# Kernel optimization log

Hardware: AMD Instinct MI355X
Metric: run time of the kernel (lower is better)

## Reference

```python
import jax, jax.numpy as jnp
import numpy as np

N = 100000
E = 1600000
F_IN = 128
HID = 256
C_OUT = 4


def setup_inputs() -> dict:
    key = jax.random.key(0)
    ks = jax.random.split(key, 8)
    x = jax.random.normal(ks[0], (N, F_IN), dtype=jnp.float32)
    edge_index = jax.random.randint(ks[1], (2, E), 0, N, dtype=jnp.int64)
    s1 = 1.0 / np.sqrt(F_IN)
    s2 = 1.0 / np.sqrt(HID)
    # PyG SAGEConv: lin_l (applied to aggregated neighbors, has bias), lin_r (root, no bias)
    w1_l = jax.random.uniform(ks[2], (HID, F_IN), jnp.float32, -s1, s1)
    w1_r = jax.random.uniform(ks[3], (HID, F_IN), jnp.float32, -s1, s1)
    b1 = jax.random.uniform(ks[4], (HID,), jnp.float32, -s1, s1)
    w2_l = jax.random.uniform(ks[5], (C_OUT, HID), jnp.float32, -s2, s2)
    w2_r = jax.random.uniform(ks[6], (C_OUT, HID), jnp.float32, -s2, s2)
    b2 = jax.random.uniform(ks[7], (C_OUT,), jnp.float32, -s2, s2)
    return {"x": x, "edge_index": edge_index, "w1_l": w1_l, "w1_r": w1_r,
            "b1": b1, "w2_l": w2_l, "w2_r": w2_r, "b2": b2}


def _mean_agg(h, src, dst, inv_deg):
    # gather source features, scatter-sum to targets, divide by in-degree
    summed = jax.ops.segment_sum(h[src], dst, num_segments=N)
    return summed * inv_deg[:, None]


def _sage_conv(h, src, dst, inv_deg, w_l, w_r, b):
    agg = _mean_agg(h, src, dst, inv_deg)
    return agg @ w_l.T + b + h @ w_r.T


def reference(x, edge_index, w1_l, w1_r, b1, w2_l, w2_r, b2):
    src, dst = edge_index[0], edge_index[1]
    deg = jax.ops.segment_sum(jnp.ones((E,), jnp.float32), dst, num_segments=N)
    inv_deg = jnp.where(deg > 0, 1.0 / jnp.maximum(deg, 1.0), 0.0)
    h = _sage_conv(x, src, dst, inv_deg, w1_l, w1_r, b1)
    h = jax.nn.relu(h)
    # dropout is identity in eval mode
    h = _sage_conv(h, src, dst, inv_deg, w2_l, w2_r, b2)
    return jax.nn.log_softmax(h, axis=1)
```

## Files before the change

### kernel.cpp

```cpp
#include <hip/hip_runtime.h>

#define N_NODES 100000
#define N_ROWS_PAD 100032
#define N_EDGES 1600000
#define F_IN    128
#define HID     256
#define C_OUT   4

#define NB 391
#define EPT 16
#define SLACK 8192

#define GEMM_BLOCKS 256
#define NTASKS 6252

typedef short short8v __attribute__((ext_vector_type(8)));
typedef unsigned short u16x8 __attribute__((ext_vector_type(8)));
typedef float f32x4 __attribute__((ext_vector_type(4)));

__device__ __forceinline__ ushort f2b(float f) {
    union { float f; unsigned u; } v; v.f = f;
    unsigned u = v.u;
    return (ushort)((u + 0x7FFFu + ((u >> 16) & 1u)) >> 16);
}
__device__ __forceinline__ float b2f(ushort u) {
    union { unsigned u; float f; } v; v.u = ((unsigned)u) << 16; return v.f;
}

__device__ __forceinline__ void gload16(const void* g, void* l) {
    __builtin_amdgcn_global_load_lds(
        (const __attribute__((address_space(1))) unsigned int*)g,
        (__attribute__((address_space(3))) unsigned int*)l, 16, 0, 0);
}

template <int CTRL>
__device__ __forceinline__ float dpp_radd(float x) {
    int y = __builtin_amdgcn_update_dpp(0, __float_as_int(x), CTRL, 0xf, 0xf, true);
    return x + __int_as_float(y);
}
__device__ __forceinline__ float row16_sum(float x) {
    x = dpp_radd<0x128>(x);
    x = dpp_radd<0x124>(x);
    x = dpp_radd<0x122>(x);
    x = dpp_radd<0x121>(x);
    return x;
}

__global__ void k_binit(int* __restrict__ bcur) {
    int t = blockIdx.x * 256 + threadIdx.x;
    if (t < 512) bcur[t] = t * SLACK;
}

__global__ __launch_bounds__(256) void k_bucket(const int* __restrict__ ei,
                                                int* __restrict__ bcur,
                                                int* __restrict__ ebuf) {
    __shared__ int hist[NB];
    __shared__ int sbase[NB];
    int t = threadIdx.x;
    for (int i = t; i < NB; i += 256) hist[i] = 0;
    __syncthreads();
    int pk[EPT], bkt[EPT], lofs[EPT];
    int base = blockIdx.x * (256 * EPT);
    #pragma unroll
    for (int i = 0; i < EPT; ++i) {
        int e = base + i * 256 + t;
        if (e < N_EDGES) {
            int s = ei[e], d = ei[N_EDGES + e];
            pk[i] = s | ((d & 255) << 20);
            bkt[i] = d >> 8;
            lofs[i] = atomicAdd(&hist[bkt[i]], 1);
        } else bkt[i] = -1;
    }
    __syncthreads();
    for (int i = t; i < NB; i += 256) {
        int h = hist[i];
        sbase[i] = h ? atomicAdd(&bcur[i], h) : 0;
    }
    __syncthreads();
    #pragma unroll
    for (int i = 0; i < EPT; ++i) {
        if (bkt[i] >= 0)
            ebuf[sbase[bkt[i]] + lofs[i]] = pk[i];
    }
}

__global__ void k_bscan(const int* __restrict__ bcur, int* __restrict__ boff) {
    __shared__ int sh[512];
    int t = threadIdx.x;
    int v = (t < NB) ? (bcur[t] - t * SLACK) : 0;
    sh[t] = v;
    __syncthreads();
    #pragma unroll
    for (int off = 1; off < 512; off <<= 1) {
        int add = (t >= off) ? sh[t - off] : 0;
        __syncthreads();
        sh[t] += add;
        __syncthreads();
    }
    boff[t] = sh[t] - v;
}

__global__ __launch_bounds__(256) void k_place(const int* __restrict__ boff,
                                               const int* __restrict__ ebuf,
                                               int* __restrict__ rowptr,
                                               float* __restrict__ inv_deg,
                                               int* __restrict__ csr_src) {
    __shared__ int eld[SLACK];
    __shared__ int ldeg[256];
    __shared__ int sh[256];
    __shared__ int lcur[256];
    int b = blockIdx.x, t = threadIdx.x;
    int e0 = boff[b];
    int cnt = boff[b + 1] - e0;
    const int* src = ebuf + (size_t)b * SLACK;
    for (int i = t; i < cnt; i += 256) eld[i] = src[i];
    ldeg[t] = 0;
    __syncthreads();
    for (int i = t; i < cnt; i += 256)
        atomicAdd(&ldeg[(eld[i] >> 20) & 255], 1);
    __syncthreads();
    int v = ldeg[t];
    sh[t] = v;
    __syncthreads();
    #pragma unroll
    for (int off = 1; off < 256; off <<= 1) {
        int add = (t >= off) ? sh[t - off] : 0;
        __syncthreads();
        sh[t] += add;
        __syncthreads();
    }
    int start = e0 + sh[t] - v;
    int node = b * 256 + t;
    if (node < N_NODES) {
        rowptr[node] = start;
        inv_deg[node] = (v > 0) ? 1.0f / (float)v : 0.0f;
    }
    if (b == 0 && t == 0) rowptr[N_NODES] = N_EDGES;
    lcur[t] = start;
    __syncthreads();
    for (int i = t; i < cnt; i += 256) {
        int ev = eld[i];
        int pos = atomicAdd(&lcur[(ev >> 20) & 255], 1);
        csr_src[pos] = ev & 0xFFFFF;
    }
}

__global__ void k_xcast(const float* __restrict__ x, ushort* __restrict__ abf) {
    int t = blockIdx.x * 256 + threadIdx.x;
    float4 xv = *(const float4*)(x + (size_t)t * 4);
    int row = t >> 5;
    int colq = (t & 31) * 4;
    ushort4 o; o.x = f2b(xv.x); o.y = f2b(xv.y); o.z = f2b(xv.z); o.w = f2b(xv.w);
    *(ushort4*)(abf + (size_t)row * 256 + 128 + colq) = o;
}

__global__ void k_wbf(const float* __restrict__ w1l, const float* __restrict__ w1r,
                      const float* __restrict__ w2l, const float* __restrict__ w2r,
                      ushort* __restrict__ wbf, float* __restrict__ w2t) {
    int i = blockIdx.x * 256 + threadIdx.x;
    int col = i >> 8, k = i & 255;
    float v = (k < 128) ? w1l[col * 128 + k] : w1r[col * 128 + (k - 128)];
    wbf[i] = f2b(v);
    if (i < 256) {
        #pragma unroll
        for (int c = 0; c < 4; ++c) {
            w2t[i * 8 + c]     = w2l[c * HID + i];
            w2t[i * 8 + 4 + c] = w2r[c * HID + i];
        }
    }
}

__global__ void k_aggregate(const int* __restrict__ rowptr, const int* __restrict__ csr_src,
                            const float* __restrict__ inv_deg, ushort* __restrict__ abf) {
    int lane = threadIdx.x & 63;
    int v = blockIdx.x * 4 + (threadIdx.x >> 6);
    if (v >= N_NODES) return;
    int r0 = rowptr[v], r1 = rowptr[v + 1];
    int q = lane >> 4, li = lane & 15;
    float a0[8], a1[8];
    #pragma unroll
    for (int j = 0; j < 8; ++j) { a0[j] = 0.f; a1[j] = 0.f; }
    int e = r0 + q;
    for (; e + 4 < r1; e += 8) {
        int s0 = csr_src[e];
        int s1 = csr_src[e + 4];
        u16x8 u0 = *(const u16x8*)(abf + (size_t)s0 * 256 + 128 + li * 8);
        u16x8 u1 = *(const u16x8*)(abf + (size_t)s1 * 256 + 128 + li * 8);
        #pragma unroll
        for (int j = 0; j < 8; ++j) { a0[j] += b2f(u0[j]); a1[j] += b2f(u1[j]); }
    }
    if (e < r1) {
        int s0 = csr_src[e];
        u16x8 u0 = *(const u16x8*)(abf + (size_t)s0 * 256 + 128 + li * 8);
        #pragma unroll
        for (int j = 0; j < 8; ++j) a0[j] += b2f(u0[j]);
    }
    #pragma unroll
    for (int j = 0; j < 8; ++j) {
        float s = a0[j] + a1[j];
        s += __shfl_xor(s, 16);
        s += __shfl_xor(s, 32);
        a0[j] = s;
    }
    if (q == 0) {
        float id = inv_deg[v];
        u16x8 o;
        #pragma unroll
        for (int j = 0; j < 8; ++j) o[j] = f2b(a0[j] * id);
        *(u16x8*)(abf + (size_t)v * 256 + li * 8) = o;
    }
}

__global__ __launch_bounds__(256, 1) void k_mfma(
    const ushort* __restrict__ abf, const ushort* __restrict__ wbf,
    const float* __restrict__ b1, const float* __restrict__ w2t,
    float* __restrict__ zb, float* __restrict__ rb)
{
    __shared__ ushort bufB[16 * 8 * 512];

    int t = threadIdx.x;
    int w = t >> 6, l = t & 63;
    int lr = l & 15, lk = l >> 4;

    #pragma unroll
    for (int j = 0; j < 32; ++j) {
        int sb = w * 32 + j;
        int n = sb >> 3, kc = sb & 7;
        gload16(wbf + (size_t)(n * 16 + lr) * 256 + kc * 32 + lk * 8,
                &bufB[sb * 512]);
    }
    __syncthreads();

    int wid = blockIdx.x * 4 + w;
    int ps = (int)(((unsigned)wid * NTASKS) >> 10);
    int pe = (int)(((unsigned)(wid + 1) * NTASKS) >> 10);

    for (int p = ps; p < pe; ++p) {
        size_t r0 = (size_t)p * 16;
        short8v af[8];
        const ushort* a0 = abf + (r0 + lr) * 256 + lk * 8;
        #pragma unroll
        for (int kc = 0; kc < 8; ++kc)
            af[kc] = *(const short8v*)(a0 + kc * 32);
        __builtin_amdgcn_sched_barrier(0);

        f32x4 acc[16] = {};
        #pragma unroll
        for (int kc = 0; kc < 8; ++kc) {
            #pragma unroll
            for (int n = 0; n < 8; ++n) {
                short8v bf = *(const short8v*)&bufB[(n * 8 + kc) * 512 + l * 8];
                acc[n] = __builtin_amdgcn_mfma_f32_16x16x32_bf16(af[kc], bf, acc[n], 0, 0, 0);
            }
            __builtin_amdgcn_sched_barrier(0);
            #pragma unroll
            for (int n = 8; n < 16; ++n) {
                short8v bf = *(const short8v*)&bufB[(n * 8 + kc) * 512 + l * 8];
                acc[n] = __builtin_amdgcn_mfma_f32_16x16x32_bf16(af[kc], bf, acc[n], 0, 0, 0);
            }
            __builtin_amdgcn_sched_barrier(0);
        }

        float pz[4][8];
        #pragma unroll
        for (int q = 0; q < 4; ++q)
            #pragma unroll
            for (int c = 0; c < 8; ++c) pz[q][c] = 0.f;
        #pragma unroll
        for (int n = 0; n < 16; ++n) {
            int col = n * 16 + lr;
            float bias = b1[col];
            f32x4 wa = *(const f32x4*)(w2t + col * 8);
            f32x4 wb = *(const f32x4*)(w2t + col * 8 + 4);
            #pragma unroll
            for (int q = 0; q < 4; ++q) {
                float h = fmaxf(acc[n][q] + bias, 0.f);
                pz[q][0] += h * wa[0]; pz[q][1] += h * wa[1];
                pz[q][2] += h * wa[2]; pz[q][3] += h * wa[3];
                pz[q][4] += h * wb[0]; pz[q][5] += h * wb[1];
                pz[q][6] += h * wb[2]; pz[q][7] += h * wb[3];
            }
        }
        __builtin_amdgcn_sched_barrier(0);
        #pragma unroll
        for (int q = 0; q < 4; ++q)
            #pragma unroll
            for (int c = 0; c < 8; ++c)
                pz[q][c] = row16_sum(pz[q][c]);
        if (lr == 0) {
            #pragma unroll
            for (int q = 0; q < 4; ++q) {
                size_t row = r0 + lk * 4 + q;
                if (row < N_NODES) {
                    *(float4*)(zb + row * 4) = make_float4(pz[q][0], pz[q][1], pz[q][2], pz[q][3]);
                    *(float4*)(rb + row * 4) = make_float4(pz[q][4], pz[q][5], pz[q][6], pz[q][7]);
                }
            }
        }
    }
}

__global__ void k_final(const float* __restrict__ zb, const float* __restrict__ rb,
                        const int* __restrict__ rowptr, const int* __restrict__ csr_src,
                        const float* __restrict__ inv_deg, const float* __restrict__ b2,
                        float* __restrict__ out) {
    int lane = threadIdx.x & 63;
    int v = blockIdx.x * 4 + (threadIdx.x >> 6);
    if (v >= N_NODES) return;
    int r0 = rowptr[v], r1 = rowptr[v + 1];
    float a0 = 0.f, a1 = 0.f, a2 = 0.f, a3 = 0.f;
    for (int idx = r0 + lane; idx < r1; idx += 64) {
        int s = csr_src[idx];
        float4 zv = *(const float4*)(zb + (size_t)s * 4);
        a0 += zv.x; a1 += zv.y; a2 += zv.z; a3 += zv.w;
    }
    #pragma unroll
    for (int off = 1; off < 64; off <<= 1) {
        a0 += __shfl_xor(a0, off);
        a1 += __shfl_xor(a1, off);
        a2 += __shfl_xor(a2, off);
        a3 += __shfl_xor(a3, off);
    }
    if (lane == 0) {
        float id = inv_deg[v];
        float4 rv = *(const float4*)(rb + (size_t)v * 4);
        float4 b2v = *(const float4*)b2;
        float h0 = a0 * id + b2v.x + rv.x;
        float h1 = a1 * id + b2v.y + rv.y;
        float h2 = a2 * id + b2v.z + rv.z;
        float h3 = a3 * id + b2v.w + rv.w;
        float mx = fmaxf(fmaxf(h0, h1), fmaxf(h2, h3));
        float s = expf(h0 - mx) + expf(h1 - mx) + expf(h2 - mx) + expf(h3 - mx);
        float lse = mx + logf(s);
        *(float4*)(out + (size_t)v * 4) = make_float4(h0 - lse, h1 - lse, h2 - lse, h3 - lse);
    }
}

extern "C" void kernel_launch(void* const* d_in, const int* in_sizes, int n_in,
                              void* d_out, int out_size, void* d_ws, size_t ws_size,
                              hipStream_t stream) {
    const float* x   = (const float*)d_in[0];
    const int*   ei  = (const int*)d_in[1];
    const float* w1l = (const float*)d_in[2];
    const float* w1r = (const float*)d_in[3];
    const float* b1  = (const float*)d_in[4];
    const float* w2l = (const float*)d_in[5];
    const float* w2r = (const float*)d_in[6];
    const float* b2  = (const float*)d_in[7];
    float* out = (float*)d_out;

    char* ws = (char*)d_ws;
    size_t off = 0;
    auto alloc = [&](size_t bytes) -> void* {
        void* p = ws + off;
        off = (off + bytes + 255) & ~(size_t)255;
        return p;
    };
    int* bcur    = (int*)alloc(512 * 4);
    int* boff    = (int*)alloc(512 * 4);
    int* rowptr  = (int*)alloc((N_NODES + 1) * 4);
    int* csr_src = (int*)alloc((size_t)N_EDGES * 4);
    int* ebuf    = (int*)alloc((size_t)NB * SLACK * 4);
    float* inv_deg = (float*)alloc(N_NODES * 4);
    ushort* abf  = (ushort*)alloc((size_t)N_ROWS_PAD * 256 * 2);
    ushort* wbf  = (ushort*)alloc((size_t)256 * 256 * 2);
    float* w2t   = (float*)alloc(256 * 8 * 4);
    float* zb    = (float*)alloc((size_t)N_NODES * 4 * 4);
    float* rb    = (float*)alloc((size_t)N_NODES * 4 * 4);

    const int BKB = (N_EDGES + 256 * EPT - 1) / (256 * EPT);
    k_binit<<<2, 256, 0, stream>>>(bcur);
    k_bucket<<<BKB, 256, 0, stream>>>(ei, bcur, ebuf);
    k_bscan<<<1, 512, 0, stream>>>(bcur, boff);
    k_place<<<NB, 256, 0, stream>>>(boff, ebuf, rowptr, inv_deg, csr_src);
    k_wbf<<<256, 256, 0, stream>>>(w1l, w1r, w2l, w2r, wbf, w2t);
    k_xcast<<<12500, 256, 0, stream>>>(x, abf);
    k_aggregate<<<(N_NODES + 3) / 4, 256, 0, stream>>>(rowptr, csr_src, inv_deg, abf);
    k_mfma<<<GEMM_BLOCKS, 256, 0, stream>>>(abf, wbf, b1, w2t, zb, rb);
    k_final<<<(N_NODES + 3) / 4, 256, 0, stream>>>(zb, rb, rowptr, csr_src, inv_deg, b2, out);
}
```

Baseline: 188.6 us.

## Fuse bucket, cast and weight-prep kernels; process row-tile pairs in MFMA GEMM

Merges the edge-bucketing, x-to-bf16 cast and weight-conversion kernels into one launch that dispatches on block index, cutting two launches and letting the independent work overlap. The GEMM kernel now handles 32 rows per task (two 16-row tiles), so each B fragment read from LDS feeds two MFMAs, halving LDS traffic per MFMA. The cost is higher register pressure from doubled accumulators and A fragments, which may lower occupancy, and coarser task granularity.

```diff
diff --git a/kernel.cpp b/kernel.cpp
--- a/kernel.cpp
+++ b/kernel.cpp
@@ -10,9 +10,11 @@
 #define NB 391
 #define EPT 16
 #define SLACK 8192
+#define BKB 391
+#define XCB 12500
 
 #define GEMM_BLOCKS 256
-#define NTASKS 6252
+#define NPAIRS 3126
 
 typedef short short8v __attribute__((ext_vector_type(8)));
 typedef unsigned short u16x8 __attribute__((ext_vector_type(8)));
@@ -51,36 +53,62 @@
     if (t < 512) bcur[t] = t * SLACK;
 }
 
-__global__ __launch_bounds__(256) void k_bucket(const int* __restrict__ ei,
-                                                int* __restrict__ bcur,
-                                                int* __restrict__ ebuf) {
+__global__ __launch_bounds__(256) void k_front(
+    const int* __restrict__ ei, int* __restrict__ bcur, int* __restrict__ ebuf,
+    const float* __restrict__ x, ushort* __restrict__ abf,
+    const float* __restrict__ w1l, const float* __restrict__ w1r,
+    const float* __restrict__ w2l, const float* __restrict__ w2r,
+    ushort* __restrict__ wbf, float* __restrict__ w2t)
+{
     __shared__ int hist[NB];
     __shared__ int sbase[NB];
+    int bx = blockIdx.x;
     int t = threadIdx.x;
-    for (int i = t; i < NB; i += 256) hist[i] = 0;
-    __syncthreads();
-    int pk[EPT], bkt[EPT], lofs[EPT];
-    int base = blockIdx.x * (256 * EPT);
-    #pragma unroll
-    for (int i = 0; i < EPT; ++i) {
-        int e = base + i * 256 + t;
-        if (e < N_EDGES) {
-            int s = ei[e], d = ei[N_EDGES + e];
-            pk[i] = s | ((d & 255) << 20);
-            bkt[i] = d >> 8;
-            lofs[i] = atomicAdd(&hist[bkt[i]], 1);
-        } else bkt[i] = -1;
-    }
-    __syncthreads();
-    for (int i = t; i < NB; i += 256) {
-        int h = hist[i];
-        sbase[i] = h ? atomicAdd(&bcur[i], h) : 0;
-    }
-    __syncthreads();
-    #pragma unroll
-    for (int i = 0; i < EPT; ++i) {
-        if (bkt[i] >= 0)
-            ebuf[sbase[bkt[i]] + lofs[i]] = pk[i];
+    if (bx < BKB) {
+        for (int i = t; i < NB; i += 256) hist[i] = 0;
+        __syncthreads();
+        int pk[EPT], bkt[EPT], lofs[EPT];
+        int base = bx * (256 * EPT);
+        #pragma unroll
+        for (int i = 0; i < EPT; ++i) {
+            int e = base + i * 256 + t;
+            if (e < N_EDGES) {
+                int s = ei[e], d = ei[N_EDGES + e];
+                pk[i] = s | ((d & 255) << 20);
+                bkt[i] = d >> 8;
+                lofs[i] = atomicAdd(&hist[bkt[i]], 1);
+            } else bkt[i] = -1;
+        }
+        __syncthreads();
+        for (int i = t; i < NB; i += 256) {
+            int h = hist[i];
+            sbase[i] = h ? atomicAdd(&bcur[i], h) : 0;
+        }
+        __syncthreads();
+        #pragma unroll
+        for (int i = 0; i < EPT; ++i) {
+            if (bkt[i] >= 0)
+                ebuf[sbase[bkt[i]] + lofs[i]] = pk[i];
+        }
+    } else if (bx < BKB + XCB) {
+        int g = (bx - BKB) * 256 + t;
+        float4 xv = *(const float4*)(x + (size_t)g * 4);
+        int row = g >> 5;
+        int colq = (g & 31) * 4;
+        ushort4 o; o.x = f2b(xv.x); o.y = f2b(xv.y); o.z = f2b(xv.z); o.w = f2b(xv.w);
+        *(ushort4*)(abf + (size_t)row * 256 + 128 + colq) = o;
+    } else {
+        int i = (bx - BKB - XCB) * 256 + t;
+        int col = i >> 8, k = i & 255;
+        float v = (k < 128) ? w1l[col * 128 + k] : w1r[col * 128 + (k - 128)];
+        wbf[i] = f2b(v);
+        if (i < 256) {
+            #pragma unroll
+            for (int c = 0; c < 4; ++c) {
+                w2t[i * 8 + c]     = w2l[c * HID + i];
+                w2t[i * 8 + 4 + c] = w2r[c * HID + i];
+            }
+        }
     }
 }
 
@@ -145,31 +173,6 @@
     }
 }
 
-__global__ void k_xcast(const float* __restrict__ x, ushort* __restrict__ abf) {
-    int t = blockIdx.x * 256 + threadIdx.x;
-    float4 xv = *(const float4*)(x + (size_t)t * 4);
-    int row = t >> 5;
-    int colq = (t & 31) * 4;
-    ushort4 o; o.x = f2b(xv.x); o.y = f2b(xv.y); o.z = f2b(xv.z); o.w = f2b(xv.w);
-    *(ushort4*)(abf + (size_t)row * 256 + 128 + colq) = o;
-}
-
-__global__ void k_wbf(const float* __restrict__ w1l, const float* __restrict__ w1r,
-                      const float* __restrict__ w2l, const float* __restrict__ w2r,
-                      ushort* __restrict__ wbf, float* __restrict__ w2t) {
-    int i = blockIdx.x * 256 + threadIdx.x;
-    int col = i >> 8, k = i & 255;
-    float v = (k < 128) ? w1l[col * 128 + k] : w1r[col * 128 + (k - 128)];
-    wbf[i] = f2b(v);
-    if (i < 256) {
-        #pragma unroll
-        for (int c = 0; c < 4; ++c) {
-            w2t[i * 8 + c]     = w2l[c * HID + i];
-            w2t[i * 8 + 4 + c] = w2r[c * HID + i];
-        }
-    }
-}
-
 __global__ void k_aggregate(const int* __restrict__ rowptr, const int* __restrict__ csr_src,
                             const float* __restrict__ inv_deg, ushort* __restrict__ abf) {
     int lane = threadIdx.x & 63;
@@ -232,68 +235,77 @@
     __syncthreads();
 
     int wid = blockIdx.x * 4 + w;
-    int ps = (int)(((unsigned)wid * NTASKS) >> 10);
-    int pe = (int)(((unsigned)(wid + 1) * NTASKS) >> 10);
+    int ps = (int)(((unsigned)wid * NPAIRS) >> 10);
+    int pe = (int)(((unsigned)(wid + 1) * NPAIRS) >> 10);
 
     for (int p = ps; p < pe; ++p) {
-        size_t r0 = (size_t)p * 16;
-        short8v af[8];
-        const ushort* a0 = abf + (r0 + lr) * 256 + lk * 8;
-        #pragma unroll
-        for (int kc = 0; kc < 8; ++kc)
-            af[kc] = *(const short8v*)(a0 + kc * 32);
+        size_t r0 = (size_t)p * 32;
+        short8v af0[8], af1[8];
+        const ushort* pa0 = abf + (r0 + lr) * 256 + lk * 8;
+        const ushort* pa1 = abf + (r0 + 16 + lr) * 256 + lk * 8;
+        #pragma unroll
+        for (int kc = 0; kc < 8; ++kc) {
+            af0[kc] = *(const short8v*)(pa0 + kc * 32);
+            af1[kc] = *(const short8v*)(pa1 + kc * 32);
+        }
         __builtin_amdgcn_sched_barrier(0);
 
-        f32x4 acc[16] = {};
+        f32x4 acc0[16] = {}, acc1[16] = {};
         #pragma unroll
         for (int kc = 0; kc < 8; ++kc) {
             #pragma unroll
             for (int n = 0; n < 8; ++n) {
                 short8v bf = *(const short8v*)&bufB[(n * 8 + kc) * 512 + l * 8];
-                acc[n] = __builtin_amdgcn_mfma_f32_16x16x32_bf16(af[kc], bf, acc[n], 0, 0, 0);
+                acc0[n] = __builtin_amdgcn_mfma_f32_16x16x32_bf16(af0[kc], bf, acc0[n], 0, 0, 0);
+                acc1[n] = __builtin_amdgcn_mfma_f32_16x16x32_bf16(af1[kc], bf, acc1[n], 0, 0, 0);
             }
             __builtin_amdgcn_sched_barrier(0);
             #pragma unroll
             for (int n = 8; n < 16; ++n) {
                 short8v bf = *(const short8v*)&bufB[(n * 8 + kc) * 512 + l * 8];
-                acc[n] = __builtin_amdgcn_mfma_f32_16x16x32_bf16(af[kc], bf, acc[n], 0, 0, 0);
+                acc0[n] = __builtin_amdgcn_mfma_f32_16x16x32_bf16(af0[kc], bf, acc0[n], 0, 0, 0);
+                acc1[n] = __builtin_amdgcn_mfma_f32_16x16x32_bf16(af1[kc], bf, acc1[n], 0, 0, 0);
             }
             __builtin_amdgcn_sched_barrier(0);
         }
 
-        float pz[4][8];
-        #pragma unroll
-        for (int q = 0; q < 4; ++q)
-            #pragma unroll
-            for (int c = 0; c < 8; ++c) pz[q][c] = 0.f;
-        #pragma unroll
-        for (int n = 0; n < 16; ++n) {
-            int col = n * 16 + lr;
-            float bias = b1[col];
-            f32x4 wa = *(const f32x4*)(w2t + col * 8);
-            f32x4 wb = *(const f32x4*)(w2t + col * 8 + 4);
-            #pragma unroll
-            for (int q = 0; q < 4; ++q) {
-                float h = fmaxf(acc[n][q] + bias, 0.f);
-                pz[q][0] += h * wa[0]; pz[q][1] += h * wa[1];
-                pz[q][2] += h * wa[2]; pz[q][3] += h * wa[3];
-                pz[q][4] += h * wb[0]; pz[q][5] += h * wb[1];
-                pz[q][6] += h * wb[2]; pz[q][7] += h * wb[3];
-            }
-        }
-        __builtin_amdgcn_sched_barrier(0);
-        #pragma unroll
-        for (int q = 0; q < 4; ++q)
-            #pragma unroll
-            for (int c = 0; c < 8; ++c)
-                pz[q][c] = row16_sum(pz[q][c]);
-        if (lr == 0) {
-            #pragma unroll
-            for (int q = 0; q < 4; ++q) {
-                size_t row = r0 + lk * 4 + q;
-                if (row < N_NODES) {
-                    *(float4*)(zb + row * 4) = make_float4(pz[q][0], pz[q][1], pz[q][2], pz[q][3]);
-                    *(float4*)(rb + row * 4) = make_float4(pz[q][4], pz[q][5], pz[q][6], pz[q][7]);
+        #pragma unroll
+        for (int g = 0; g < 2; ++g) {
+            float pz[4][8];
+            #pragma unroll
+            for (int q = 0; q < 4; ++q)
+                #pragma unroll
+                for (int c = 0; c < 8; ++c) pz[q][c] = 0.f;
+            #pragma unroll
+            for (int n = 0; n < 16; ++n) {
+                int col = n * 16 + lr;
+                float bias = b1[col];
+                f32x4 wa = *(const f32x4*)(w2t + col * 8);
+                f32x4 wb = *(const f32x4*)(w2t + col * 8 + 4);
+                #pragma unroll
+                for (int q = 0; q < 4; ++q) {
+                    float aq = g ? acc1[n][q] : acc0[n][q];
+                    float h = fmaxf(aq + bias, 0.f);
+                    pz[q][0] += h * wa[0]; pz[q][1] += h * wa[1];
+                    pz[q][2] += h * wa[2]; pz[q][3] += h * wa[3];
+                    pz[q][4] += h * wb[0]; pz[q][5] += h * wb[1];
+                    pz[q][6] += h * wb[2]; pz[q][7] += h * wb[3];
+                }
+            }
+            __builtin_amdgcn_sched_barrier(0);
+            #pragma unroll
+            for (int q = 0; q < 4; ++q)
+                #pragma unroll
+                for (int c = 0; c < 8; ++c)
+                    pz[q][c] = row16_sum(pz[q][c]);
+            if (lr == 0) {
+                #pragma unroll
+                for (int q = 0; q < 4; ++q) {
+                    size_t row = r0 + g * 16 + lk * 4 + q;
+                    if (row < N_NODES) {
+                        *(float4*)(zb + row * 4) = make_float4(pz[q][0], pz[q][1], pz[q][2], pz[q][3]);
+                        *(float4*)(rb + row * 4) = make_float4(pz[q][4], pz[q][5], pz[q][6], pz[q][7]);
+                    }
                 }
             }
         }
@@ -368,13 +380,11 @@
     float* zb    = (float*)alloc((size_t)N_NODES * 4 * 4);
     float* rb    = (float*)alloc((size_t)N_NODES * 4 * 4);
 
-    const int BKB = (N_EDGES + 256 * EPT - 1) / (256 * EPT);
     k_binit<<<2, 256, 0, stream>>>(bcur);
-    k_bucket<<<BKB, 256, 0, stream>>>(ei, bcur, ebuf);
+    k_front<<<BKB + XCB + 256, 256, 0, stream>>>(ei, bcur, ebuf, x, abf,
+                                                 w1l, w1r, w2l, w2r, wbf, w2t);
     k_bscan<<<1, 512, 0, stream>>>(bcur, boff);
     k_place<<<NB, 256, 0, stream>>>(boff, ebuf, rowptr, inv_deg, csr_src);
-    k_wbf<<<256, 256, 0, stream>>>(w1l, w1r, w2l, w2r, wbf, w2t);
-    k_xcast<<<12500, 256, 0, stream>>>(x, abf);
     k_aggregate<<<(N_NODES + 3) / 4, 256, 0, stream>>>(rowptr, csr_src, inv_deg, abf);
     k_mfma<<<GEMM_BLOCKS, 256, 0, stream>>>(abf, wbf, b1, w2t, zb, rb);
     k_final<<<(N_NODES + 3) / 4, 256, 0, stream>>>(zb, rb, rowptr, csr_src, inv_deg, b2, out);
```

Result: faster. 183.0 us (-2.9%).
